# Kernel optimization log

Hardware: AMD Instinct MI355X
Metric: run time of the kernel (lower is better)

## Reference

```python
import jax, jax.numpy as jnp
import numpy as np
from jax import lax

B, T, C, U = 32, 512, 4233, 64


def setup_inputs() -> dict:
    key = jax.random.key(0)
    k1, k2 = jax.random.split(key)
    logits = jax.random.normal(k1, (B, T, C), dtype=jnp.float32)
    ctc_logit = jax.nn.log_softmax(logits, axis=-1)  # [B, T, C] log-probs
    # labels in [1, C) so none equal blank (code treats blank-valued labels as pad)
    label = jax.random.randint(k2, (U, B), 1, C, dtype=jnp.int32)  # [U, B]
    return {"ctc_logit": ctc_logit, "label": label, "blank_id": 0}


def ctc_fa(ctc_logit, label, blank_id):
    pad_value = jnp.finfo(ctc_logit.dtype).min
    lab = label.T  # [B, U]
    lab = jnp.where(lab == blank_id, -1, lab)
    Bb, Uu = lab.shape
    Tt = ctc_logit.shape[1]
    Cc = ctc_logit.shape[2]
    yl = (lab >= 0).sum(1) * 2 + 1  # [B] extended label length
    # interleave blanks: [blank, l0, blank, l1, ..., blank] -> lab_T = 2U+1
    blanks = jnp.full_like(lab, blank_id)
    ext = jnp.stack([blanks, lab], axis=2).reshape(Bb, 2 * Uu)
    ext = jnp.pad(ext, ((0, 0), (0, 1)), constant_values=blank_id)  # [B, labT]
    labT = 2 * Uu + 1
    shifted2 = jnp.pad(ext, ((0, 0), (2, 0)), constant_values=-1)[:, :labT]
    cond = (ext == blank_id) | (ext == shifted2)  # [B, labT]
    ext_idx = ext % Cc  # mimic torch negative-index wrap for -1 pad labels
    # emission log-probs gathered per extended-label position: [B, T, labT]
    emit = jnp.take_along_axis(ctc_logit, ext_idx[:, None, :], axis=2)
    dp0 = jnp.full((Bb, labT), pad_value, ctc_logit.dtype)
    dp0 = dp0.at[:, 0].set(emit[:, 0, 0]).at[:, 1].set(emit[:, 0, 1])
    jrange = jnp.arange(labT)

    def shift(x, n):
        return jnp.pad(x, ((0, 0), (n, 0)), constant_values=pad_value)[:, :labT]

    def step(dp_prev, emit_t):
        s1 = shift(dp_prev, 1)
        s2 = shift(dp_prev, 2)
        a2 = jnp.stack([dp_prev, s1], axis=-1)          # [B, labT, 2]
        a3 = jnp.stack([dp_prev, s1, s2], axis=-1)      # [B, labT, 3]
        idx1 = jnp.argmax(a2, axis=-1)
        idx2 = jnp.argmax(a3, axis=-1)
        lse2 = jax.scipy.special.logsumexp(a2, axis=-1)
        lse3 = jax.scipy.special.logsumexp(a3, axis=-1)
        dp_t = emit_t + jnp.where(cond, lse2, lse3)
        bp_t = jrange[None, :] - jnp.where(cond, idx1, idx2)
        return dp_t, (dp_t, bp_t)

    emit_tbj = jnp.swapaxes(emit, 0, 1)  # [T, B, labT]
    dp_last, (_, bps) = lax.scan(step, dp0, emit_tbj[1:])
    bp0 = jnp.broadcast_to(jrange[None, None, :], (1, Bb, labT)).astype(bps.dtype)
    bp_all = jnp.concatenate([bp0, bps], axis=0)  # [T, B, labT]
    bi = jnp.arange(Bb)
    d1 = dp_last[bi, yl - 1]
    d2 = dp_last[bi, yl - 2]
    ctc_loss = -jnp.logaddexp(d1, d2)
    ctc_loss = 2 * ctc_loss / (yl - 1)
    # Viterbi backtrack -> hard alignment [B, T, labT]
    wi0 = jnp.where(d1 > d2, yl - 1, yl - 2)

    def bstep(wi, bp_t):
        align_t = (jrange[None, :] == wi[:, None]).astype(jnp.int32)
        wi_next = jnp.take_along_axis(bp_t, wi[:, None], axis=1)[:, 0]
        return wi_next, align_t

    _, align_ts = lax.scan(bstep, wi0, bp_all, reverse=True)  # [T, B, labT]
    align = jnp.swapaxes(align_ts, 0, 1)  # [B, T, labT]
    return align, ctc_loss


def reference(ctc_logit, label, blank_id):
    return ctc_fa(ctc_logit, label, blank_id)
```

## Files before the change

### kernel.cpp

```cpp
#include <hip/hip_runtime.h>
#include <math.h>

#define NB 32
#define NT 512
#define NC 4233
#define NU 64
#define LABT 129
#define PADV (-3.4028234663852886e38f)
#define EMITP_N (NB * NT * 128)

__global__ __launch_bounds__(256)
void ctc_gather_kernel(const float* __restrict__ logit,
                       const int*   __restrict__ label,
                       const int*   __restrict__ blank_ptr,
                       float*       __restrict__ emitP)
{
    int tid = blockIdx.x * 256 + threadIdx.x;
    if (tid >= EMITP_N) return;
    int bt = tid >> 7;
    int j  = tid & 127;
    int b  = bt / NT;
    int blank = blank_ptr[0];
    int col;
    if (j & 1) {
        int raw = label[((j - 1) >> 1) * NB + b];
        int ev  = (raw == blank) ? -1 : raw;
        col = ev % NC;
        if (col < 0) col += NC;
    } else {
        col = blank;
    }
    emitP[tid] = logit[(size_t)bt * NC + col];
}

__device__ __forceinline__ float dpp_wave_shr1(float x, float fill) {
    return __int_as_float(__builtin_amdgcn_update_dpp(
        __float_as_int(fill), __float_as_int(x), 0x138 ,
        0xf, 0xf, false));
}

__global__ __launch_bounds__(64)
void ctc_scan_kernel(const float* __restrict__ emitP,
                     const int*   __restrict__ label,
                     const int*   __restrict__ blank_ptr,
                     float* __restrict__ out,
                     float* __restrict__ loss_out)
{
    __shared__ __align__(16) unsigned long long bpm[NT][4];
    __shared__ int   wl[NT];
    __shared__ float fdp[132];

    const int b = blockIdx.x;
    const int l = threadIdx.x;
    const int blank = blank_ptr[0];

    int raw = label[l * NB + b];
    unsigned long long nbmask = __ballot(raw != blank);
    const int Y = 2 * (int)__popcll(nbmask) + 1;
    int ev  = (raw == blank) ? -1 : raw;
    int pev = __shfl_up(ev, 1);
    if (l == 0) pev = -1;
    const bool cndO = (ev == blank) || (ev == pev);

    const float2* ep = (const float2*)(emitP + (size_t)b * NT * 128) + l;

    float2 e00 = ep[0];
    float v0 = (l == 0) ? e00.x : PADV;
    float v1 = (l == 0) ? e00.y : PADV;
    float v2 = PADV;

    float2 r0 = ep[1 * 64], r1 = ep[2 * 64], r2 = ep[3 * 64], r3 = ep[4 * 64];
    float2 r4 = ep[5 * 64], r5 = ep[6 * 64], r6 = ep[7 * 64], r7 = ep[8 * 64];

#define STEP(tcur, rr, tload)                                                  \
    do {                                                                       \
        float u1 = dpp_wave_shr1(v1, PADV);                      \
                              \
        float mE   = fmaxf(v0, u1);                                            \
        float lseE = mE + logf(1.0f + expf(-fabsf(v0 - u1)));                  \
        unsigned long long bE = __ballot(v0 < u1);                             \
                     \
        float c2e = cndO ? PADV : u1;                                          \
        float mO  = fmaxf(fmaxf(v1, v0), c2e);                                 \
        float lseO = mO + logf(expf(v1 - mO) + expf(v0 - mO) + expf(c2e - mO));\
        unsigned long long gAB = __ballot(v1 >= v0);                           \
        unsigned long long gAC = __ballot(v1 >= c2e);                          \
        unsigned long long gBC = __ballot(v0 >= c2e);                          \
                                    \
        float mL   = fmaxf(v2, v1);                                            \
        float lseL = mL + logf(1.0f + expf(-fabsf(v2 - v1)));                  \
        unsigned long long bL = __ballot(v2 < v1);                             \
                            \
        float eL = __int_as_float(                                             \
            __builtin_amdgcn_readfirstlane(__float_as_int(rr.x)));             \
        v0 = rr.x + lseE;                                                      \
        v1 = rr.y + lseO;                                                      \
        v2 = eL   + lseL;                                                      \
        if (l == 0) {                                                          \
            unsigned long long t0m = gAB & gAC;                                \
            bpm[tcur][0] = bE;                                                 \
            bpm[tcur][1] = ~t0m & gBC;                                         \
            bpm[tcur][2] = ~t0m & ~gBC;                                        \
            bpm[tcur][3] = (bL >> 63);                                         \
        }                                                                      \
        if ((tload) < NT) rr = ep[(tload) * 64];                               \
    } while (0)

    int t = 1;
    for (; t + 7 < NT; t += 8) {
        STEP(t,     r0, t + 8);
        STEP(t + 1, r1, t + 9);
        STEP(t + 2, r2, t + 10);
        STEP(t + 3, r3, t + 11);
        STEP(t + 4, r4, t + 12);
        STEP(t + 5, r5, t + 13);
        STEP(t + 6, r6, t + 14);
        STEP(t + 7, r7, t + 15);
    }
    STEP(t,     r0, NT);
    STEP(t + 1, r1, NT);
    STEP(t + 2, r2, NT);
    STEP(t + 3, r3, NT);
    STEP(t + 4, r4, NT);
    STEP(t + 5, r5, NT);
    STEP(t + 6, r6, NT);
#undef STEP

    fdp[2 * l]     = v0;
    fdp[2 * l + 1] = v1;
    if (l == 63) fdp[128] = v2;
    __syncthreads();

    float* outA = out + (size_t)b * (NT * LABT);
    {
        float4 z4; z4.x = 0.f; z4.y = 0.f; z4.z = 0.f; z4.w = 0.f;
        float4* o4 = (float4*)outA;
        for (int p = l; p < (NT * LABT) / 4; p += 64) o4[p] = z4;
    }

    if (l == 0) {
        int i2 = Y - 2; if (i2 < 0) i2 += LABT;
        float d1 = fdp[Y - 1];
        float d2 = fdp[i2];
        float mm = fmaxf(d1, d2);
        float la = mm + logf(expf(d1 - mm) + expf(d2 - mm));
        loss_out[b] = -la * 2.0f / (float)(Y - 1);

        int w = (d1 > d2) ? (Y - 1) : i2;
        const ulonglong2* bp2 = (const ulonglong2*)&bpm[0][0];

#define BLOAD(qa, qb, row) do { qa = bp2[2 * (row)]; qb = bp2[2 * (row) + 1]; } while (0)
#define BPROC(qa, qb, row) do {                                                \
        wl[row] = w;                                                           \
        int lw_ = w >> 1;                                                      \
        int dE_ = (w == 128) ? (int)qb.y : (int)((qa.x >> lw_) & 1ULL);        \
        int dO_ = (int)((qa.y >> lw_) & 1ULL) + 2 * (int)((qb.x >> lw_) & 1ULL);\
        w -= (w & 1) ? dO_ : dE_;                                              \
    } while (0)

        ulonglong2 a0, b0, a1, b1, a2, b2, a3, b3;
        BLOAD(a0, b0, NT - 1);
        BLOAD(a1, b1, NT - 2);
        BLOAD(a2, b2, NT - 3);
        BLOAD(a3, b3, NT - 4);
        int tt;
        for (tt = NT - 1; tt >= 8; tt -= 4) {
            BPROC(a0, b0, tt    ); BLOAD(a0, b0, tt - 4);
            BPROC(a1, b1, tt - 1); BLOAD(a1, b1, tt - 5);
            BPROC(a2, b2, tt - 2); BLOAD(a2, b2, tt - 6);
            BPROC(a3, b3, tt - 3); BLOAD(a3, b3, tt - 7);
        }
        BPROC(a0, b0, 7); BLOAD(a0, b0, 3);
        BPROC(a1, b1, 6); BLOAD(a1, b1, 2);
        BPROC(a2, b2, 5); BLOAD(a2, b2, 1);
        BPROC(a3, b3, 4);
        BPROC(a0, b0, 3);
        BPROC(a1, b1, 2);
        BPROC(a2, b2, 1);
        wl[0] = w;
#undef BLOAD
#undef BPROC
    }
    __syncthreads();

    for (int t2 = l; t2 < NT; t2 += 64)
        outA[(size_t)t2 * LABT + wl[t2]] = 1.0f;
}

extern "C" void kernel_launch(void* const* d_in, const int* in_sizes, int n_in,
                              void* d_out, int out_size, void* d_ws, size_t ws_size,
                              hipStream_t stream)
{
    const float* logit = (const float*)d_in[0];
    const int*   label = (const int*)d_in[1];
    const int*   blank = (const int*)d_in[2];

    float* out = (float*)d_out;

    float* emitP = (float*)d_ws;

    ctc_gather_kernel<<<EMITP_N / 256, 256, 0, stream>>>(
        logit, label, blank, emitP);
    ctc_scan_kernel<<<NB, 64, 0, stream>>>(
        emitP, label, blank, out, out + (size_t)NB * NT * LABT);
}
```

Baseline: 542.3 us.

## Stage emission rows into LDS via async global_load_lds double buffering

The scan kernel now streams each batch's emission rows into a 64KB double-buffered LDS staging area using global_load_lds in 32KB chunks, waiting on vmcnt before each chunk. The recurrence then reads rows from LDS with a 4-deep register prefetch instead of issuing a global load every step. The backpointer stores are also merged into two 16-byte writes. The aim is to take global memory latency off the serial time recurrence, at the cost of extra LDS use and more complex wait/synchronisation logic.

```diff
diff --git a/kernel.cpp b/kernel.cpp
--- a/kernel.cpp
+++ b/kernel.cpp
@@ -8,6 +8,9 @@
 #define LABT 129
 #define PADV (-3.4028234663852886e38f)
 #define EMITP_N (NB * NT * 128)
+
+typedef __attribute__((address_space(3))) unsigned int lu32;
+typedef __attribute__((address_space(1))) unsigned int gu32;
 
 __global__ __launch_bounds__(256)
 void ctc_gather_kernel(const float* __restrict__ logit,
@@ -46,6 +49,7 @@
                      float* __restrict__ out,
                      float* __restrict__ loss_out)
 {
+    __shared__ __align__(16) char stage[65536];
     __shared__ __align__(16) unsigned long long bpm[NT][4];
     __shared__ int   wl[NT];
     __shared__ float fdp[132];
@@ -62,24 +66,49 @@
     if (l == 0) pev = -1;
     const bool cndO = (ev == blank) || (ev == pev);
 
-    const float2* ep = (const float2*)(emitP + (size_t)b * NT * 128) + l;
-
-    float2 e00 = ep[0];
+    const char* gbase = (const char*)(emitP + (size_t)b * NT * 128);
+
+#define STAGE_CHUNK(k)                                                         \
+    do {                                                                       \
+        const char* gsrc_ = gbase + (size_t)(k) * 32768 + l * 16;              \
+        char* ldst_ = stage + (((k) & 1) << 15);                               \
+        _Pragma("unroll")                                                      \
+        for (int i_ = 0; i_ < 32; ++i_) {                                      \
+            __builtin_amdgcn_global_load_lds(                                  \
+                (const gu32*)(gsrc_ + i_ * 1024),                              \
+                (lu32*)(ldst_ + i_ * 1024), 16, 0, 0);                         \
+        }                                                                      \
+    } while (0)
+
+#define WAITVM(n)                                                              \
+    do { asm volatile("s_waitcnt vmcnt(" #n ")" ::: "memory");                 \
+         __builtin_amdgcn_sched_barrier(0); } while (0)
+#define WAITLGKM0                                                              \
+    do { asm volatile("s_waitcnt lgkmcnt(0)" ::: "memory");                    \
+         __builtin_amdgcn_sched_barrier(0); } while (0)
+
+#define ROWPTR(p) ((const float2*)(stage + ((((p) >> 6) & 1) << 15)            \
+                                         + (((p) & 63) << 9)) + l)
+
+    STAGE_CHUNK(0);
+    STAGE_CHUNK(1);
+    WAITVM(32);
+
+    float2 e00 = *ROWPTR(0);
     float v0 = (l == 0) ? e00.x : PADV;
     float v1 = (l == 0) ? e00.y : PADV;
     float v2 = PADV;
 
-    float2 r0 = ep[1 * 64], r1 = ep[2 * 64], r2 = ep[3 * 64], r3 = ep[4 * 64];
-    float2 r4 = ep[5 * 64], r5 = ep[6 * 64], r6 = ep[7 * 64], r7 = ep[8 * 64];
-
-#define STEP(tcur, rr, tload)                                                  \
+    float2 q1 = *ROWPTR(1), q2 = *ROWPTR(2), q3 = *ROWPTR(3), q0 = *ROWPTR(4);
+
+#define STEPL(t_, rr)                                                          \
     do {                                                                       \
         float u1 = dpp_wave_shr1(v1, PADV);                      \
                               \
         float mE   = fmaxf(v0, u1);                                            \
         float lseE = mE + logf(1.0f + expf(-fabsf(v0 - u1)));                  \
         unsigned long long bE = __ballot(v0 < u1);                             \
-                     \
+                      \
         float c2e = cndO ? PADV : u1;                                          \
         float mO  = fmaxf(fmaxf(v1, v0), c2e);                                 \
         float lseO = mO + logf(expf(v1 - mO) + expf(v0 - mO) + expf(c2e - mO));\
@@ -98,33 +127,30 @@
         v2 = eL   + lseL;                                                      \
         if (l == 0) {                                                          \
             unsigned long long t0m = gAB & gAC;                                \
-            bpm[tcur][0] = bE;                                                 \
-            bpm[tcur][1] = ~t0m & gBC;                                         \
-            bpm[tcur][2] = ~t0m & ~gBC;                                        \
-            bpm[tcur][3] = (bL >> 63);                                         \
+            ulonglong2 w01, w23;                                               \
+            w01.x = bE;          w01.y = ~t0m & gBC;                           \
+            w23.x = ~t0m & ~gBC; w23.y = (bL >> 63);                           \
+            *(ulonglong2*)&bpm[t_][0] = w01;                                   \
+            *(ulonglong2*)&bpm[t_][2] = w23;                                   \
         }                                                                      \
-        if ((tload) < NT) rr = ep[(tload) * 64];                               \
+        rr = *ROWPTR((t_) + 4);          \
     } while (0)
 
-    int t = 1;
-    for (; t + 7 < NT; t += 8) {
-        STEP(t,     r0, t + 8);
-        STEP(t + 1, r1, t + 9);
-        STEP(t + 2, r2, t + 10);
-        STEP(t + 3, r3, t + 11);
-        STEP(t + 4, r4, t + 12);
-        STEP(t + 5, r5, t + 13);
-        STEP(t + 6, r6, t + 14);
-        STEP(t + 7, r7, t + 15);
-    }
-    STEP(t,     r0, NT);
-    STEP(t + 1, r1, NT);
-    STEP(t + 2, r2, NT);
-    STEP(t + 3, r3, NT);
-    STEP(t + 4, r4, NT);
-    STEP(t + 5, r5, NT);
-    STEP(t + 6, r6, NT);
-#undef STEP
+    STEPL(1, q1); STEPL(2, q2); STEPL(3, q3);
+    for (int tb = 4; tb < 60; tb += 4) {
+        STEPL(tb, q0); STEPL(tb + 1, q1); STEPL(tb + 2, q2); STEPL(tb + 3, q3);
+    }
+    for (int c = 0; c < 7; ++c) {
+        WAITLGKM0;
+        WAITVM(0);
+        if (c < 6) STAGE_CHUNK(c + 2);
+        const int base = 60 + (c << 6);
+        for (int tb = base; tb < base + 64; tb += 4) {
+            STEPL(tb, q0); STEPL(tb + 1, q1); STEPL(tb + 2, q2); STEPL(tb + 3, q3);
+        }
+    }
+    STEPL(508, q0); STEPL(509, q1); STEPL(510, q2); STEPL(511, q3);
+#undef STEPL
 
     fdp[2 * l]     = v0;
     fdp[2 * l + 1] = v1;
```

New measurement: 566.1 us. 1.04x slower.

## Split emissions into label and blank streams and double-buffer scan prefetch

Applied to the files above, without the earlier changes.

The gather kernel now writes label emissions as float4 packs of four timesteps per lane and stores the blank emission once per timestep in a separate array, instead of duplicating blank values across the interleaved layout. The scan kernel preloads blank emissions per 64-step block and broadcasts them with readlane. It also double-buffers 16 float4 loads ahead per block, replacing the previous 8-step rolling register prefetch. The aim is to cut redundant workspace traffic and hide global load latency on the serial recurrence, at the cost of much higher register pressure from the 32 float4 buffers.

```diff
diff --git a/kernel.cpp b/kernel.cpp
--- a/kernel.cpp
+++ b/kernel.cpp
@@ -7,30 +7,42 @@
 #define NU 64
 #define LABT 129
 #define PADV (-3.4028234663852886e38f)
-#define EMITP_N (NB * NT * 128)
 
 __global__ __launch_bounds__(256)
 void ctc_gather_kernel(const float* __restrict__ logit,
                        const int*   __restrict__ label,
                        const int*   __restrict__ blank_ptr,
-                       float*       __restrict__ emitP)
+                       float4*      __restrict__ oddS,
+                       float*       __restrict__ blankS)
 {
     int tid = blockIdx.x * 256 + threadIdx.x;
-    if (tid >= EMITP_N) return;
-    int bt = tid >> 7;
-    int j  = tid & 127;
-    int b  = bt / NT;
+    int l   = tid & 63;
+    int bt4 = tid >> 6;
+    int b   = bt4 >> 7;
+    int t4  = bt4 & 127;
     int blank = blank_ptr[0];
-    int col;
-    if (j & 1) {
-        int raw = label[((j - 1) >> 1) * NB + b];
-        int ev  = (raw == blank) ? -1 : raw;
-        col = ev % NC;
-        if (col < 0) col += NC;
-    } else {
-        col = blank;
+
+    int raw = label[l * NB + b];
+    int ev  = (raw == blank) ? -1 : raw;
+    int col = ev % NC;
+    if (col < 0) col += NC;
+
+    const float* lg = logit + ((size_t)b * NT + (size_t)t4 * 4) * NC;
+    float4 o;
+    o.x = lg[col];
+    o.y = lg[NC + col];
+    o.z = lg[2 * NC + col];
+    o.w = lg[3 * NC + col];
+    oddS[(size_t)bt4 * 64 + l] = o;
+
+    if (l == 0) {
+        float4 bl;
+        bl.x = lg[blank];
+        bl.y = lg[NC + blank];
+        bl.z = lg[2 * NC + blank];
+        bl.w = lg[3 * NC + blank];
+        *(float4*)&blankS[(size_t)b * NT + t4 * 4] = bl;
     }
-    emitP[tid] = logit[(size_t)bt * NC + col];
 }
 
 __device__ __forceinline__ float dpp_wave_shr1(float x, float fill) {
@@ -39,10 +51,11 @@
         0xf, 0xf, false));
 }
 
-__global__ __launch_bounds__(64)
-void ctc_scan_kernel(const float* __restrict__ emitP,
-                     const int*   __restrict__ label,
-                     const int*   __restrict__ blank_ptr,
+__global__ __launch_bounds__(64, 1)
+void ctc_scan_kernel(const float4* __restrict__ oddS,
+                     const float*  __restrict__ blankS,
+                     const int*    __restrict__ label,
+                     const int*    __restrict__ blank_ptr,
                      float* __restrict__ out,
                      float* __restrict__ loss_out)
 {
@@ -62,24 +75,30 @@
     if (l == 0) pev = -1;
     const bool cndO = (ev == blank) || (ev == pev);
 
-    const float2* ep = (const float2*)(emitP + (size_t)b * NT * 128) + l;
-
-    float2 e00 = ep[0];
-    float v0 = (l == 0) ? e00.x : PADV;
-    float v1 = (l == 0) ? e00.y : PADV;
+    const float4* ep4 = oddS + (size_t)b * 128 * 64;
+    const float*  bS  = blankS + (size_t)b * NT;
+
+    float bv0 = bS[l],       bv1 = bS[64 + l],  bv2 = bS[128 + l],
+          bv3 = bS[192 + l], bv4 = bS[256 + l], bv5 = bS[320 + l],
+          bv6 = bS[384 + l], bv7 = bS[448 + l];
+
+    float4 bufA[16], bufB[16];
+#pragma unroll
+    for (int q = 0; q < 16; ++q) bufA[q] = ep4[q * 64 + l];
+    __builtin_amdgcn_sched_barrier(0);
+
+    float v0 = (l == 0) ? bv0 : PADV;
+    float v1 = (l == 0) ? bufA[0].x : PADV;
     float v2 = PADV;
 
-    float2 r0 = ep[1 * 64], r1 = ep[2 * 64], r2 = ep[3 * 64], r3 = ep[4 * 64];
-    float2 r4 = ep[5 * 64], r5 = ep[6 * 64], r6 = ep[7 * 64], r7 = ep[8 * 64];
-
-#define STEP(tcur, rr, tload)                                                  \
+#define STEP_T(t_, evv, se)                                                    \
     do {                                                                       \
         float u1 = dpp_wave_shr1(v1, PADV);                      \
                               \
         float mE   = fmaxf(v0, u1);                                            \
         float lseE = mE + logf(1.0f + expf(-fabsf(v0 - u1)));                  \
         unsigned long long bE = __ballot(v0 < u1);                             \
-                     \
+                      \
         float c2e = cndO ? PADV : u1;                                          \
         float mO  = fmaxf(fmaxf(v1, v0), c2e);                                 \
         float lseO = mO + logf(expf(v1 - mO) + expf(v0 - mO) + expf(c2e - mO));\
@@ -90,41 +109,48 @@
         float mL   = fmaxf(v2, v1);                                            \
         float lseL = mL + logf(1.0f + expf(-fabsf(v2 - v1)));                  \
         unsigned long long bL = __ballot(v2 < v1);                             \
-                            \
-        float eL = __int_as_float(                                             \
-            __builtin_amdgcn_readfirstlane(__float_as_int(rr.x)));             \
-        v0 = rr.x + lseE;                                                      \
-        v1 = rr.y + lseO;                                                      \
-        v2 = eL   + lseL;                                                      \
+        v0 = (se) + lseE;                                                      \
+        v1 = (evv) + lseO;                                                     \
+        v2 = (se) + lseL;                                                      \
         if (l == 0) {                                                          \
             unsigned long long t0m = gAB & gAC;                                \
-            bpm[tcur][0] = bE;                                                 \
-            bpm[tcur][1] = ~t0m & gBC;                                         \
-            bpm[tcur][2] = ~t0m & ~gBC;                                        \
-            bpm[tcur][3] = (bL >> 63);                                         \
+            ulonglong2 w01, w23;                                               \
+            w01.x = bE;          w01.y = ~t0m & gBC;                           \
+            w23.x = ~t0m & ~gBC; w23.y = (bL >> 63);                           \
+            *(ulonglong2*)&bpm[t_][0] = w01;                                   \
+            *(ulonglong2*)&bpm[t_][2] = w23;                                   \
         }                                                                      \
-        if ((tload) < NT) rr = ep[(tload) * 64];                               \
     } while (0)
 
-    int t = 1;
-    for (; t + 7 < NT; t += 8) {
-        STEP(t,     r0, t + 8);
-        STEP(t + 1, r1, t + 9);
-        STEP(t + 2, r2, t + 10);
-        STEP(t + 3, r3, t + 11);
-        STEP(t + 4, r4, t + 12);
-        STEP(t + 5, r5, t + 13);
-        STEP(t + 6, r6, t + 14);
-        STEP(t + 7, r7, t + 15);
-    }
-    STEP(t,     r0, NT);
-    STEP(t + 1, r1, NT);
-    STEP(t + 2, r2, NT);
-    STEP(t + 3, r3, NT);
-    STEP(t + 4, r4, NT);
-    STEP(t + 5, r5, NT);
-    STEP(t + 6, r6, NT);
-#undef STEP
+#define BLOCK64(base, CUR, NXT, BV, DO_PREFETCH)                               \
+    do {                                                                       \
+        if (DO_PREFETCH) {                                                     \
+            _Pragma("unroll")                                                  \
+            for (int q = 0; q < 16; ++q)                                       \
+                NXT[q] = ep4[(((base) >> 2) + 16 + q) * 64 + l];               \
+            __builtin_amdgcn_sched_barrier(0);                                 \
+        }                                                                      \
+        _Pragma("unroll")                                                      \
+        for (int i = ((base) == 0 ? 1 : 0); i < 64; ++i) {                     \
+            float4 cc = CUR[i >> 2];                                           \
+            float evv = ((i & 3) == 0) ? cc.x : ((i & 3) == 1) ? cc.y          \
+                      : ((i & 3) == 2) ? cc.z : cc.w;                          \
+            float se = __int_as_float(__builtin_amdgcn_readlane(               \
+                __float_as_int(BV), i));                                       \
+            STEP_T((base) + i, evv, se);                                       \
+        }                                                                      \
+    } while (0)
+
+    BLOCK64(0,   bufA, bufB, bv0, 1);
+    BLOCK64(64,  bufB, bufA, bv1, 1);
+    BLOCK64(128, bufA, bufB, bv2, 1);
+    BLOCK64(192, bufB, bufA, bv3, 1);
+    BLOCK64(256, bufA, bufB, bv4, 1);
+    BLOCK64(320, bufB, bufA, bv5, 1);
+    BLOCK64(384, bufA, bufB, bv6, 1);
+    BLOCK64(448, bufB, bufA, bv7, 0);
+#undef BLOCK64
+#undef STEP_T
 
     fdp[2 * l]     = v0;
     fdp[2 * l + 1] = v1;
@@ -197,10 +223,11 @@
 
     float* out = (float*)d_out;
 
-    float* emitP = (float*)d_ws;
-
-    ctc_gather_kernel<<<EMITP_N / 256, 256, 0, stream>>>(
-        logit, label, blank, emitP);
+    float4* oddS   = (float4*)d_ws;
+    float*  blankS = (float*)((char*)d_ws + (size_t)NB * 128 * 64 * 16);
+
+    ctc_gather_kernel<<<(NB * 128 * 64) / 256, 256, 0, stream>>>(
+        logit, label, blank, oddS, blankS);
     ctc_scan_kernel<<<NB, 64, 0, stream>>>(
-        emitP, label, blank, out, out + (size_t)NB * NT * LABT);
-}
+        oddS, blankS, label, blank, out, out + (size_t)NB * NT * LABT);
+}
```

Result: slower. 594.4 us (+9.6%).
